# Performance work log

Hardware: AMD Instinct MI355X
Metric: run time of the kernel (lower is better)

## Reference

```python
import jax, jax.numpy as jnp
import numpy as np

N, M, K, D, H, C = 100000, 10000, 32, 64, 8, 64


def setup_inputs() -> dict:
    key = jax.random.key(0)
    ks = jax.random.split(key, 7)
    x = jax.random.normal(ks[0], (N, D), dtype=jnp.float32)
    src_idx = jax.random.randint(ks[1], (M, K), 0, N)
    dst_idx = jax.random.randint(ks[2], (M,), 0, N)
    # Linear weights stored as [in, out] (y = x @ W), matching torch Linear math
    Wq = jax.random.normal(ks[3], (D, D), dtype=jnp.float32) / np.sqrt(D)
    Wk = jax.random.normal(ks[4], (D, D * H), dtype=jnp.float32) / np.sqrt(D)
    Wp1 = jax.random.normal(ks[5], (H, H), dtype=jnp.float32) / np.sqrt(H)
    Wp2 = jax.random.normal(ks[6], (H, C), dtype=jnp.float32) / np.sqrt(H)
    return {"x": x, "src_idx": src_idx, "dst_idx": dst_idx,
            "Wq": Wq, "Wk": Wk, "Wp1": Wp1, "Wp2": Wp2}


def reference(x, src_idx, dst_idx, Wq, Wk, Wp1, Wp2):
    # gather destination / source node features (irregular access)
    n_i = x[dst_idx] @ Wq                              # [M, D]
    n_j = (x[src_idx] @ Wk).reshape(M, K, H, D)        # [M, K, H, D]
    # multi-head QK pair score, scaled by sqrt(dim)
    pair = jnp.einsum('md,mkhd->mkh', n_i, n_j) / jnp.sqrt(jnp.asarray(D, x.dtype))
    # small MLP head (dropout in eval mode = identity)
    hidden = jax.nn.relu(pair @ Wp1)                   # [M, K, H]
    logits = (hidden @ Wp2).reshape(M * K, C)          # [M*K, C]
    return logits
```

## Files before the change

kernel.cpp:

```cpp
#include <hip/hip_runtime.h>


#define Mm 10000
#define Kk 32
#define Dd 64
#define Hh 8
#define Cc 64

constexpr int MA = 16;
constexpr size_t A_BYTES = (size_t)Mm * Hh * Dd * sizeof(float);

__global__ __launch_bounds__(256) void disto_A(
    const float* __restrict__ x,
    const int*   __restrict__ dst_idx,
    const float* __restrict__ Wq,
    const float* __restrict__ Wk,
    float* __restrict__ A)
{
    __shared__ float xs[MA][68];
    __shared__ float ni[MA][68];
    __shared__ float wk[Dd][68];

    const int t  = threadIdx.x;
    const int m0 = blockIdx.x * MA;
    const int h  = blockIdx.y;
    const int mi = t >> 4;
    const int j  = t & 15;

    {
        int idx = dst_idx[m0 + mi];
        float4 v = ((const float4*)x)[(size_t)idx * 16 + j];
        *(float4*)&xs[mi][j * 4] = v;
    }
    #pragma unroll
    for (int p = 0; p < 4; ++p) {
        int task = p * 256 + t;
        int dp = task >> 4;
        int q  = task & 15;
        float4 v = ((const float4*)Wk)[(size_t)dp * 128 + h * 16 + q];
        *(float4*)&wk[dp][q * 4] = v;
    }
    __syncthreads();

    {
        float4 acc = make_float4(0.f, 0.f, 0.f, 0.f);
        #pragma unroll
        for (int d = 0; d < Dd; ++d) {
            float  xv = xs[mi][d];
            float4 wv = ((const float4*)Wq)[d * 16 + j];
            acc.x = fmaf(xv, wv.x, acc.x);
            acc.y = fmaf(xv, wv.y, acc.y);
            acc.z = fmaf(xv, wv.z, acc.z);
            acc.w = fmaf(xv, wv.w, acc.w);
        }
        *(float4*)&ni[mi][j * 4] = acc;
    }
    __syncthreads();

    float res[4];
    #pragma unroll
    for (int rep = 0; rep < 4; ++rep) {
        const int dp = rep * 16 + j;
        const float4* wr = (const float4*)wk[dp];
        const float4* nr = (const float4*)ni[mi];
        float acc = 0.f;
        #pragma unroll
        for (int d4 = 0; d4 < 16; ++d4) {
            float4 nv = nr[d4];
            float4 wv = wr[d4];
            acc = fmaf(nv.x, wv.x, acc);
            acc = fmaf(nv.y, wv.y, acc);
            acc = fmaf(nv.z, wv.z, acc);
            acc = fmaf(nv.w, wv.w, acc);
        }
        res[rep] = acc * 0.125f;
    }
    #pragma unroll
    for (int rep = 0; rep < 4; ++rep)
        A[(size_t)(m0 + mi) * 512 + h * 64 + rep * 16 + j] = res[rep];
}

__global__ __launch_bounds__(256) void disto_B(
    const float* __restrict__ x,
    const int*   __restrict__ src_idx,
    const float* __restrict__ A,
    const float* __restrict__ Wp1,
    const float* __restrict__ Wp2,
    float* __restrict__ out)
{
    __shared__ float a_lds[Hh][68];
    __shared__ float xs[Kk][68];
    __shared__ float wp2[Hh * Cc];

    const int t = threadIdx.x;
    const int m = blockIdx.x;
    const int w = t >> 6;
    const int l = t & 63;

    if (t < 128) {
        float4 v = ((const float4*)A)[(size_t)m * 128 + t];
        *(float4*)&a_lds[t >> 4][(t & 15) * 4] = v;
    } else {
        ((float4*)wp2)[t - 128] = ((const float4*)Wp2)[t - 128];
    }
    #pragma unroll
    for (int p = 0; p < 2; ++p) {
        int task = p * 256 + t;
        int r = task >> 4;
        int q = task & 15;
        int idx = src_idx[m * Kk + r];
        float4 v = ((const float4*)x)[(size_t)idx * 16 + q];
        *(float4*)&xs[r][q * 4] = v;
    }

    const int h_role = l & 7;
    const int k8     = l >> 3;
    float wp1r[8];
    #pragma unroll
    for (int jj = 0; jj < 8; ++jj) wp1r[jj] = Wp1[h_role * Hh + jj];

    __syncthreads();

    const int k = w * 8 + k8;
    float pair = 0.f;
    {
        const float4* xr = (const float4*)xs[k];
        const float4* ar = (const float4*)a_lds[h_role];
        #pragma unroll
        for (int d4 = 0; d4 < 16; ++d4) {
            float4 xv = xr[d4];
            float4 av = ar[d4];
            pair = fmaf(xv.x, av.x, pair);
            pair = fmaf(xv.y, av.y, pair);
            pair = fmaf(xv.z, av.z, pair);
            pair = fmaf(xv.w, av.w, pair);
        }
    }

    float hid[8];
    #pragma unroll
    for (int jj = 0; jj < 8; ++jj) hid[jj] = pair * wp1r[jj];
    #pragma unroll
    for (int s = 1; s < 8; s <<= 1) {
        #pragma unroll
        for (int jj = 0; jj < 8; ++jj)
            hid[jj] += __shfl_xor(hid[jj], s, 64);
    }
    #pragma unroll
    for (int jj = 0; jj < 8; ++jj) hid[jj] = fmaxf(hid[jj], 0.f);

    float lg[8] = {0,0,0,0,0,0,0,0};
    #pragma unroll
    for (int hp = 0; hp < 8; ++hp) {
        const float* wrow = &wp2[hp * Cc + h_role * 8];
        float4 wa = *(const float4*)wrow;
        float4 wb = *(const float4*)(wrow + 4);
        lg[0] = fmaf(hid[hp], wa.x, lg[0]);
        lg[1] = fmaf(hid[hp], wa.y, lg[1]);
        lg[2] = fmaf(hid[hp], wa.z, lg[2]);
        lg[3] = fmaf(hid[hp], wa.w, lg[3]);
        lg[4] = fmaf(hid[hp], wb.x, lg[4]);
        lg[5] = fmaf(hid[hp], wb.y, lg[5]);
        lg[6] = fmaf(hid[hp], wb.z, lg[6]);
        lg[7] = fmaf(hid[hp], wb.w, lg[7]);
    }
    size_t row = (size_t)m * Kk + k;
    float4* o4 = (float4*)(out + row * Cc + h_role * 8);
    o4[0] = make_float4(lg[0], lg[1], lg[2], lg[3]);
    o4[1] = make_float4(lg[4], lg[5], lg[6], lg[7]);
}

constexpr int WAVES = 4;
constexpr int PAD = 68;

__global__ __launch_bounds__(256) void disto_fused(
    const float* __restrict__ x,
    const int*   __restrict__ src_idx,
    const int*   __restrict__ dst_idx,
    const float* __restrict__ Wq,
    const float* __restrict__ Wk,
    const float* __restrict__ Wp1,
    const float* __restrict__ Wp2,
    float* __restrict__ out)
{
    __shared__ float ni_lds[WAVES][Dd];
    __shared__ float A_lds[WAVES][Hh][PAD];
    __shared__ float xs_lds[WAVES][8][PAD];
    __shared__ float wp2_lds[Hh * Cc];

    const int t = threadIdx.x;
    const int w = t >> 6;
    const int l = t & 63;
    const int m = blockIdx.x * WAVES + w;

    if (t < 128) ((float4*)wp2_lds)[t] = ((const float4*)Wp2)[t];

    const int dst = dst_idx[m];
    float xd = x[(size_t)dst * Dd + l];
    float acc1 = 0.f;
    #pragma unroll
    for (int dp = 0; dp < Dd; ++dp) {
        float xv = __shfl(xd, dp, 64);
        acc1 = fmaf(xv, Wq[dp * Dd + l], acc1);
    }
    ni_lds[w][l] = acc1;
    __syncthreads();
    {
        const float4* ni4 = (const float4*)ni_lds[w];
        const float4* wkrow = (const float4*)(Wk + (size_t)l * (Dd * Hh));
        #pragma unroll
        for (int h = 0; h < Hh; ++h) {
            float a = 0.f;
            #pragma unroll
            for (int d4 = 0; d4 < Dd / 4; ++d4) {
                float4 nv = ni4[d4];
                float4 wv = wkrow[h * (Dd / 4) + d4];
                a = fmaf(nv.x, wv.x, a);
                a = fmaf(nv.y, wv.y, a);
                a = fmaf(nv.z, wv.z, a);
                a = fmaf(nv.w, wv.w, a);
            }
            A_lds[w][h][l] = a * 0.125f;
        }
    }
    const int h_role = l & 7;
    const int k8 = l >> 3;
    float wp1r[8];
    #pragma unroll
    for (int j = 0; j < 8; ++j) wp1r[j] = Wp1[h_role * Hh + j];
    __syncthreads();

    for (int kc = 0; kc < 4; ++kc) {
        #pragma unroll
        for (int p = 0; p < 2; ++p) {
            int task = p * 64 + l;
            int r = task >> 4;
            int j = task & 15;
            int idx = src_idx[m * Kk + kc * 8 + r];
            float4 v = ((const float4*)x)[(size_t)idx * (Dd / 4) + j];
            *(float4*)&xs_lds[w][r][j * 4] = v;
        }
        __syncthreads();
        float pair = 0.f;
        {
            const float4* xsr = (const float4*)xs_lds[w][k8];
            const float4* ar  = (const float4*)A_lds[w][h_role];
            #pragma unroll
            for (int d4 = 0; d4 < Dd / 4; ++d4) {
                float4 xv = xsr[d4];
                float4 av = ar[d4];
                pair = fmaf(xv.x, av.x, pair);
                pair = fmaf(xv.y, av.y, pair);
                pair = fmaf(xv.z, av.z, pair);
                pair = fmaf(xv.w, av.w, pair);
            }
        }
        float hid[8];
        #pragma unroll
        for (int j = 0; j < 8; ++j) hid[j] = pair * wp1r[j];
        #pragma unroll
        for (int s = 1; s < 8; s <<= 1) {
            #pragma unroll
            for (int j = 0; j < 8; ++j)
                hid[j] += __shfl_xor(hid[j], s, 64);
        }
        #pragma unroll
        for (int j = 0; j < 8; ++j) hid[j] = fmaxf(hid[j], 0.f);
        float lg[8] = {0,0,0,0,0,0,0,0};
        #pragma unroll
        for (int hp = 0; hp < 8; ++hp) {
            const float* wrow = &wp2_lds[hp * Cc + h_role * 8];
            float4 wa = *(const float4*)wrow;
            float4 wb = *(const float4*)(wrow + 4);
            lg[0] = fmaf(hid[hp], wa.x, lg[0]);
            lg[1] = fmaf(hid[hp], wa.y, lg[1]);
            lg[2] = fmaf(hid[hp], wa.z, lg[2]);
            lg[3] = fmaf(hid[hp], wa.w, lg[3]);
            lg[4] = fmaf(hid[hp], wb.x, lg[4]);
            lg[5] = fmaf(hid[hp], wb.y, lg[5]);
            lg[6] = fmaf(hid[hp], wb.z, lg[6]);
            lg[7] = fmaf(hid[hp], wb.w, lg[7]);
        }
        size_t row = (size_t)(m * Kk + kc * 8 + k8);
        float4* o4 = (float4*)(out + row * Cc + h_role * 8);
        o4[0] = make_float4(lg[0], lg[1], lg[2], lg[3]);
        o4[1] = make_float4(lg[4], lg[5], lg[6], lg[7]);
        __syncthreads();
    }
}

extern "C" void kernel_launch(void* const* d_in, const int* in_sizes, int n_in,
                              void* d_out, int out_size, void* d_ws, size_t ws_size,
                              hipStream_t stream) {
    const float* x       = (const float*)d_in[0];
    const int*   src_idx = (const int*)  d_in[1];
    const int*   dst_idx = (const int*)  d_in[2];
    const float* Wq      = (const float*)d_in[3];
    const float* Wk      = (const float*)d_in[4];
    const float* Wp1     = (const float*)d_in[5];
    const float* Wp2     = (const float*)d_in[6];
    float* out = (float*)d_out;

    if (ws_size >= A_BYTES) {
        float* A = (float*)d_ws;
        disto_A<<<dim3(Mm / MA, Hh), dim3(256), 0, stream>>>(x, dst_idx, Wq, Wk, A);
        disto_B<<<dim3(Mm), dim3(256), 0, stream>>>(x, src_idx, A, Wp1, Wp2, out);
    } else {
        disto_fused<<<dim3(Mm / WAVES), dim3(256), 0, stream>>>(
            x, src_idx, dst_idx, Wq, Wk, Wp1, Wp2, out);
    }
}
```

Measured before the change: 173.7 us.

## Precompute combined Wq·Wk^T weight matrix and apply it per destination node

```diff
diff --git a/kernel.cpp b/kernel.cpp
--- a/kernel.cpp
+++ b/kernel.cpp
@@ -7,77 +7,96 @@
 #define Hh 8
 #define Cc 64
 
-constexpr int MA = 16;
-constexpr size_t A_BYTES = (size_t)Mm * Hh * Dd * sizeof(float);
-
-__global__ __launch_bounds__(256) void disto_A(
+constexpr int M_PER_A2 = 20;
+constexpr size_t WC_FLOATS = 64 * 512;
+constexpr size_t A_FLOATS  = (size_t)Mm * 512;
+constexpr size_t WS_NEED   = (WC_FLOATS + A_FLOATS) * sizeof(float);
+
+__global__ __launch_bounds__(256) void wc_build(
+    const float* __restrict__ Wq,
+    const float* __restrict__ Wk,
+    float* __restrict__ WC)
+{
+    __shared__ float wq_l[16][68];
+    __shared__ float wk_l[64][68];
+
+    const int t  = threadIdx.x;
+    const int e0 = blockIdx.x * 16;
+    const int h  = blockIdx.y;
+
+    {
+        int r = t >> 4, q = t & 15;
+        float4 v = ((const float4*)Wq)[(e0 + r) * 16 + q];
+        *(float4*)&wq_l[r][q * 4] = v;
+    }
+    #pragma unroll
+    for (int p = 0; p < 4; ++p) {
+        int task = p * 256 + t;
+        int dp = task >> 4, q = task & 15;
+        float4 v = ((const float4*)Wk)[(size_t)dp * 128 + h * 16 + q];
+        *(float4*)&wk_l[dp][q * 4] = v;
+    }
+    __syncthreads();
+
+    const int dp = t & 63;
+    const int eq = t >> 6;
+
+    float4 wr[16];
+    #pragma unroll
+    for (int d4 = 0; d4 < 16; ++d4) wr[d4] = *(const float4*)&wk_l[dp][d4 * 4];
+
+    #pragma unroll
+    for (int i = 0; i < 4; ++i) {
+        const int er = eq * 4 + i;
+        float acc = 0.f;
+        #pragma unroll
+        for (int d4 = 0; d4 < 16; ++d4) {
+            float4 qv = *(const float4*)&wq_l[er][d4 * 4];
+            acc = fmaf(qv.x, wr[d4].x, acc);
+            acc = fmaf(qv.y, wr[d4].y, acc);
+            acc = fmaf(qv.z, wr[d4].z, acc);
+            acc = fmaf(qv.w, wr[d4].w, acc);
+        }
+        WC[(size_t)(e0 + er) * 512 + h * 64 + dp] = acc * 0.125f;
+    }
+}
+
+__global__ __launch_bounds__(512) void disto_A2(
     const float* __restrict__ x,
     const int*   __restrict__ dst_idx,
-    const float* __restrict__ Wq,
-    const float* __restrict__ Wk,
+    const float* __restrict__ WC,
     float* __restrict__ A)
 {
-    __shared__ float xs[MA][68];
-    __shared__ float ni[MA][68];
-    __shared__ float wk[Dd][68];
+    __shared__ float xr[M_PER_A2][68];
 
     const int t  = threadIdx.x;
-    const int m0 = blockIdx.x * MA;
-    const int h  = blockIdx.y;
-    const int mi = t >> 4;
-    const int j  = t & 15;
-
-    {
-        int idx = dst_idx[m0 + mi];
-        float4 v = ((const float4*)x)[(size_t)idx * 16 + j];
-        *(float4*)&xs[mi][j * 4] = v;
-    }
-    #pragma unroll
-    for (int p = 0; p < 4; ++p) {
-        int task = p * 256 + t;
-        int dp = task >> 4;
-        int q  = task & 15;
-        float4 v = ((const float4*)Wk)[(size_t)dp * 128 + h * 16 + q];
-        *(float4*)&wk[dp][q * 4] = v;
-    }
-    __syncthreads();
-
-    {
-        float4 acc = make_float4(0.f, 0.f, 0.f, 0.f);
-        #pragma unroll
-        for (int d = 0; d < Dd; ++d) {
-            float  xv = xs[mi][d];
-            float4 wv = ((const float4*)Wq)[d * 16 + j];
-            acc.x = fmaf(xv, wv.x, acc.x);
-            acc.y = fmaf(xv, wv.y, acc.y);
-            acc.z = fmaf(xv, wv.z, acc.z);
-            acc.w = fmaf(xv, wv.w, acc.w);
-        }
-        *(float4*)&ni[mi][j * 4] = acc;
-    }
-    __syncthreads();
-
-    float res[4];
-    #pragma unroll
-    for (int rep = 0; rep < 4; ++rep) {
-        const int dp = rep * 16 + j;
-        const float4* wr = (const float4*)wk[dp];
-        const float4* nr = (const float4*)ni[mi];
-        float acc = 0.f;
-        #pragma unroll
-        for (int d4 = 0; d4 < 16; ++d4) {
-            float4 nv = nr[d4];
-            float4 wv = wr[d4];
-            acc = fmaf(nv.x, wv.x, acc);
-            acc = fmaf(nv.y, wv.y, acc);
-            acc = fmaf(nv.z, wv.z, acc);
-            acc = fmaf(nv.w, wv.w, acc);
-        }
-        res[rep] = acc * 0.125f;
-    }
-    #pragma unroll
-    for (int rep = 0; rep < 4; ++rep)
-        A[(size_t)(m0 + mi) * 512 + h * 64 + rep * 16 + j] = res[rep];
+    const int m0 = blockIdx.x * M_PER_A2;
+
+    if (t < M_PER_A2 * 16) {
+        int r = t >> 4, q = t & 15;
+        int idx = dst_idx[m0 + r];
+        float4 v = ((const float4*)x)[(size_t)idx * 16 + q];
+        *(float4*)&xr[r][q * 4] = v;
+    }
+
+    float wc[64];
+    #pragma unroll
+    for (int e = 0; e < 64; ++e) wc[e] = WC[(size_t)e * 512 + t];
+
+    __syncthreads();
+
+    for (int mi = 0; mi < M_PER_A2; ++mi) {
+        float acc0 = 0.f, acc1 = 0.f;
+        #pragma unroll
+        for (int e4 = 0; e4 < 16; ++e4) {
+            float4 xv = *(const float4*)&xr[mi][e4 * 4];
+            acc0 = fmaf(xv.x, wc[e4 * 4 + 0], acc0);
+            acc1 = fmaf(xv.y, wc[e4 * 4 + 1], acc1);
+            acc0 = fmaf(xv.z, wc[e4 * 4 + 2], acc0);
+            acc1 = fmaf(xv.w, wc[e4 * 4 + 3], acc1);
+        }
+        A[(size_t)(m0 + mi) * 512 + t] = acc0 + acc1;
+    }
 }
 
 __global__ __launch_bounds__(256) void disto_B(
@@ -106,8 +125,7 @@
     #pragma unroll
     for (int p = 0; p < 2; ++p) {
         int task = p * 256 + t;
-        int r = task >> 4;
-        int q = task & 15;
+        int r = task >> 4, q = task & 15;
         int idx = src_idx[m * Kk + r];
         float4 v = ((const float4*)x)[(size_t)idx * 16 + q];
         *(float4*)&xs[r][q * 4] = v;
@@ -124,11 +142,11 @@
     const int k = w * 8 + k8;
     float pair = 0.f;
     {
-        const float4* xr = (const float4*)xs[k];
-        const float4* ar = (const float4*)a_lds[h_role];
+        const float4* xr4 = (const float4*)xs[k];
+        const float4* ar  = (const float4*)a_lds[h_role];
         #pragma unroll
         for (int d4 = 0; d4 < 16; ++d4) {
-            float4 xv = xr[d4];
+            float4 xv = xr4[d4];
             float4 av = ar[d4];
             pair = fmaf(xv.x, av.x, pair);
             pair = fmaf(xv.y, av.y, pair);
@@ -301,9 +319,11 @@
     const float* Wp2     = (const float*)d_in[6];
     float* out = (float*)d_out;
 
-    if (ws_size >= A_BYTES) {
-        float* A = (float*)d_ws;
-        disto_A<<<dim3(Mm / MA, Hh), dim3(256), 0, stream>>>(x, dst_idx, Wq, Wk, A);
+    if (ws_size >= WS_NEED) {
+        float* WC = (float*)d_ws;
+        float* A  = WC + WC_FLOATS;
+        wc_build<<<dim3(4, 8), dim3(256), 0, stream>>>(Wq, Wk, WC);
+        disto_A2<<<dim3(Mm / M_PER_A2), dim3(512), 0, stream>>>(x, dst_idx, WC, A);
         disto_B<<<dim3(Mm), dim3(256), 0, stream>>>(x, src_idx, A, Wp1, Wp2, out);
     } else {
         disto_fused<<<dim3(Mm / WAVES), dim3(256), 0, stream>>>(
```

After: 156.8 us. -9.7%, faster.
